# Kernel optimization log

Measured on AMD Instinct MI355X. Metric: run time of the kernel, lower is better.

The kernel has to match this reference:

```python
import jax, jax.numpy as jnp
import numpy as np

EMBED_DIM = 1024
NUM_HEADS = 16
HEAD_DIM = EMBED_DIM // NUM_HEADS


def setup_inputs() -> dict:
    key = jax.random.key(0)
    kx, kq, kk, kv, ko = jax.random.split(key, 5)
    B, S = 4, 2048
    std = 1.0 / np.sqrt(EMBED_DIM)
    x = jax.random.normal(kx, (B, S, EMBED_DIM), dtype=jnp.float32)
    # nn.Linear weights stored as [out, in]; applied as x @ W.T
    Wq = jax.random.normal(kq, (EMBED_DIM, EMBED_DIM), dtype=jnp.float32) * std
    Wk = jax.random.normal(kk, (EMBED_DIM, EMBED_DIM), dtype=jnp.float32) * std
    Wv = jax.random.normal(kv, (EMBED_DIM, EMBED_DIM), dtype=jnp.float32) * std
    Wo = jax.random.normal(ko, (EMBED_DIM, EMBED_DIM), dtype=jnp.float32) * std
    return {"x": x, "Wq": Wq, "Wk": Wk, "Wv": Wv, "Wo": Wo}


def reference(x, Wq, Wk, Wv, Wo):
    B, S, E = x.shape
    H, D = NUM_HEADS, HEAD_DIM
    scale = jnp.sqrt(jnp.float32(D))

    def proj(W):
        # x @ W.T -> (B, S, E) -> (B, H, S, D)
        return (x @ W.T).reshape(B, S, H, D).transpose(0, 2, 1, 3)

    q, k, v = proj(Wq), proj(Wk), proj(Wv)
    scores = jnp.einsum("bhsd,bhtd->bhst", q, k) / scale  # (B,H,S,S)
    causal = jnp.tril(jnp.ones((S, S), dtype=bool))
    scores = jnp.where(causal, scores, -jnp.inf)
    attn = jax.nn.softmax(scores, axis=-1)  # dropout in eval mode = identity
    out = jnp.einsum("bhst,bhtd->bhsd", attn, v)  # (B,H,S,D)
    out = out.transpose(0, 2, 1, 3).reshape(B, S, E)
    return out @ Wo.T
```

## Files before the change

kernel.cpp:

```cpp
#include <hip/hip_runtime.h>
#include <stdint.h>

#define NHEADS 16
#define EDIM   1024
#define SEQ    2048
#define BATCH  4

typedef float  floatx4 __attribute__((ext_vector_type(4)));
typedef __bf16 bf16x8  __attribute__((ext_vector_type(8)));
typedef unsigned short u16;

__device__ __forceinline__ u16 f2bf(float f) {
  union { float f; unsigned int u; } v; v.f = f;
  return (u16)((v.u + 0x7fffu + ((v.u >> 16) & 1u)) >> 16);
}

__device__ __forceinline__ unsigned int pkbf(float lo, float hi) {
  union { float f; unsigned int u; } a, c;
  a.f = lo; c.f = hi;
  return __builtin_amdgcn_perm(c.u + 0x8000u, a.u + 0x8000u, 0x07060302u);
}

__device__ __forceinline__ void gl2lds16(const u16* g, u16* l) {
  __builtin_amdgcn_global_load_lds(
      (const __attribute__((address_space(1))) unsigned int*)g,
      (__attribute__((address_space(3))) unsigned int*)l, 16, 0, 0);
}

__global__ void cvt_all(const float* __restrict__ x,  const float* __restrict__ wq,
                        const float* __restrict__ wk, const float* __restrict__ wv,
                        const float* __restrict__ wo, u16* __restrict__ xb,
                        u16* __restrict__ wqkv, u16* __restrict__ wob, float qscale) {
  const float* src; u16* dst; int n4; float sc = 1.f;
  switch (blockIdx.y) {
    case 0: src = x;  dst = xb;             n4 = 2097152; break;
    case 1: src = wq; dst = wqkv;           n4 = 262144; sc = qscale; break;
    case 2: src = wk; dst = wqkv + 1048576; n4 = 262144; break;
    case 3: src = wv; dst = wqkv + 2097152; n4 = 262144; break;
    default: src = wo; dst = wob;           n4 = 262144; break;
  }
  const int stride = gridDim.x * blockDim.x;
  for (int i = blockIdx.x * blockDim.x + threadIdx.x; i < n4; i += stride) {
    float4 f = ((const float4*)src)[i];
    uint2 o;
    o.x = pkbf(f.x * sc, f.y * sc);
    o.y = pkbf(f.z * sc, f.w * sc);
    ((uint2*)dst)[i] = o;
  }
}

template <int MODE>
__global__ __launch_bounds__(256, 2)
void gemm_tn(const u16* __restrict__ A, const u16* __restrict__ B,
             void* __restrict__ Cq, u16* __restrict__ Ck, u16* __restrict__ Cv,
             int Kdim) {
  __shared__ u16 As[128 * 64];
  __shared__ u16 Bs[128 * 64];
  const int tid  = threadIdx.x;
  const int w    = tid >> 6, lane = tid & 63;
  const int quad = lane >> 4, l15 = lane & 15;
  const int sr   = lane >> 3, sc8 = lane & 7;
  const int rowA0 = blockIdx.y * 128, rowB0 = blockIdx.x * 128;
  const int wrow  = (w >> 1) * 64,    wcol  = (w & 1) * 64;
  const int matid = (MODE == 0) ? (rowA0 >> 10) : 1;

  const floatx4 vzero = {0.f, 0.f, 0.f, 0.f};
  floatx4 acc[4][4];
#pragma unroll
  for (int mi = 0; mi < 4; ++mi)
#pragma unroll
    for (int ni = 0; ni < 4; ++ni) acc[mi][ni] = vzero;

  for (int k0 = 0; k0 < Kdim; k0 += 64) {
    __syncthreads();
#pragma unroll
    for (int i = 0; i < 4; ++i) {
      const int r = w * 32 + i * 8;
      gl2lds16(A + (size_t)(rowA0 + r + sr) * Kdim + k0 + ((sc8 ^ sr) * 8), As + r * 64);
      gl2lds16(B + (size_t)(rowB0 + r + sr) * Kdim + k0 + ((sc8 ^ sr) * 8), Bs + r * 64);
    }
    __syncthreads();
#pragma unroll
    for (int ks = 0; ks < 2; ++ks) {
      bf16x8 af[4], bfr[4];
#pragma unroll
      for (int mi = 0; mi < 4; ++mi)
        af[mi] = *(const bf16x8*)(As + (wrow + mi * 16 + l15) * 64 + (((ks * 4 + quad) ^ (l15 & 7)) * 8));
#pragma unroll
      for (int ni = 0; ni < 4; ++ni)
        bfr[ni] = *(const bf16x8*)(Bs + (wcol + ni * 16 + l15) * 64 + (((ks * 4 + quad) ^ (l15 & 7)) * 8));
      if (MODE == 0 && matid == 2) {
#pragma unroll
        for (int mi = 0; mi < 4; ++mi)
#pragma unroll
          for (int ni = 0; ni < 4; ++ni)
            acc[mi][ni] = __builtin_amdgcn_mfma_f32_16x16x32_bf16(bfr[ni], af[mi], acc[mi][ni], 0, 0, 0);
      } else {
#pragma unroll
        for (int mi = 0; mi < 4; ++mi)
#pragma unroll
          for (int ni = 0; ni < 4; ++ni)
            acc[mi][ni] = __builtin_amdgcn_mfma_f32_16x16x32_bf16(af[mi], bfr[ni], acc[mi][ni], 0, 0, 0);
      }
    }
  }

#pragma unroll
  for (int mi = 0; mi < 4; ++mi)
#pragma unroll
    for (int ni = 0; ni < 4; ++ni) {
      if (MODE == 1) {
        const int e0 = rowA0 + wrow + mi * 16 + quad * 4;
        const int s  = rowB0 + wcol + ni * 16 + l15;
        *(floatx4*)((float*)Cq + (size_t)s * 1024 + e0) = acc[mi][ni];
      } else if (matid < 2) {
        const int e0 = rowA0 + wrow + mi * 16 + quad * 4;
        const int s  = rowB0 + wcol + ni * 16 + l15;
        const int e_loc = e0 & 1023;
        u16* dst = (matid == 0) ? (u16*)Cq : Ck;
        uint2 pk;
        pk.x = pkbf(acc[mi][ni][0], acc[mi][ni][1]);
        pk.y = pkbf(acc[mi][ni][2], acc[mi][ni][3]);
        *(uint2*)(dst + (size_t)s * 1024 + e_loc) = pk;
      } else {
        const int e_loc = (rowA0 + wrow + mi * 16 + l15) & 1023;
        const int s_full = rowB0 + wcol + ni * 16 + quad * 4;
        const int bb = s_full >> 11, s_loc = s_full & 2047;
        uint2 pk;
        pk.x = pkbf(acc[mi][ni][0], acc[mi][ni][1]);
        pk.y = pkbf(acc[mi][ni][2], acc[mi][ni][3]);
        *(uint2*)(Cv + (size_t)(bb * 1024 + e_loc) * SEQ + s_loc) = pk;
      }
    }
}

__global__ __launch_bounds__(512, 4)
void attn_fwd(const u16* __restrict__ Q, const u16* __restrict__ K,
              const u16* __restrict__ Vt, u16* __restrict__ Ctx) {
  __shared__ u16 Ks[2][128 * 64];
  __shared__ u16 Vs[2][64 * 128];
  const int tid  = threadIdx.x;
  const int w    = tid >> 6, lane = tid & 63;
  const int quad = lane >> 4, l15 = lane & 15;
  const int bh = blockIdx.x, b = bh >> 4, h = bh & 15;
  const int p  = blockIdx.y;
  const int qts[2] = {p, 15 - p};
  const int kmax = qts[1];

  bf16x8 bq[2][2];
#pragma unroll
  for (int tt = 0; tt < 2; ++tt)
#pragma unroll
    for (int ks = 0; ks < 2; ++ks) {
      const int qs = qts[tt] * 128 + w * 16 + l15;
      bq[tt][ks] = *(const bf16x8*)(Q + (size_t)(b * SEQ + qs) * EDIM + h * 64 + ks * 32 + quad * 8);
    }

  const floatx4 vzero = {0.f, 0.f, 0.f, 0.f};
  floatx4 o_acc[2][4];
  float l_run[2] = {0.f, 0.f};
#pragma unroll
  for (int tt = 0; tt < 2; ++tt)
#pragma unroll
    for (int di = 0; di < 4; ++di) o_acc[tt][di] = vzero;

  const int krow = lane >> 3, kch = lane & 7;
  const int vrow = lane >> 4, vch = lane & 15;

#define STAGE_KV(buf, ktn)                                                          \
  {                                                                                 \
    _Pragma("unroll")                                                               \
    for (int ii = 0; ii < 2; ++ii) {                                                \
      const int r0 = w * 16 + ii * 8;                                               \
      const int row = r0 + krow;                                                    \
      gl2lds16(K + (size_t)(b * SEQ + (ktn) * 128 + row) * EDIM + h * 64 +          \
                   ((kch ^ (row & 7)) * 8),                                         \
               &Ks[buf][r0 * 64]);                                                  \
      const int d0 = w * 8 + ii * 4;                                                \
      const int dd = d0 + vrow;                                                     \
      gl2lds16(Vt + (size_t)(bh * 64 + dd) * SEQ + (ktn) * 128 +                    \
                   ((vch ^ (dd & 15)) * 8),                                         \
               &Vs[buf][d0 * 128]);                                                 \
    }                                                                               \
  }

  STAGE_KV(0, 0);

  for (int kt = 0; kt <= kmax; ++kt) {
    const int cur = kt & 1;
    __syncthreads();
    if (kt < kmax) STAGE_KV(cur ^ 1, kt + 1);
    const u16* Ksc = &Ks[cur][0];
    const u16* Vsc = &Vs[cur][0];

#pragma unroll
    for (int tt = 1; tt >= 0; --tt) {
      if (tt == 0 && kt > qts[0]) continue;

      floatx4 s_acc[8];
#pragma unroll
      for (int mi = 0; mi < 8; ++mi) s_acc[mi] = vzero;
#pragma unroll
      for (int ks = 0; ks < 2; ++ks) {
        bf16x8 ak[8];
#pragma unroll
        for (int mi = 0; mi < 8; ++mi)
          ak[mi] = *(const bf16x8*)(Ksc + (mi * 16 + l15) * 64 + (((ks * 4 + quad) ^ (l15 & 7)) * 8));
#pragma unroll
        for (int mi = 0; mi < 8; ++mi)
          s_acc[mi] = __builtin_amdgcn_mfma_f32_16x16x32_bf16(ak[mi], bq[tt][ks], s_acc[mi], 0, 0, 0);
      }

      if (kt == qts[tt]) {
        const int q_loc = w * 16 + l15;
#pragma unroll
        for (int mi = 0; mi < 8; ++mi)
#pragma unroll
          for (int r = 0; r < 4; ++r) {
            const int t_loc = mi * 16 + quad * 4 + r;
            if (t_loc > q_loc) s_acc[mi][r] = -1e30f;
          }
      }

      float ls = 0.f;
      unsigned int pk[4][4];
#pragma unroll
      for (int mi = 0; mi < 8; ++mi) {
        float p0 = __builtin_amdgcn_exp2f(s_acc[mi][0]);
        float p1 = __builtin_amdgcn_exp2f(s_acc[mi][1]);
        float p2 = __builtin_amdgcn_exp2f(s_acc[mi][2]);
        float p3 = __builtin_amdgcn_exp2f(s_acc[mi][3]);
        ls += (p0 + p1) + (p2 + p3);
        pk[mi >> 1][(mi & 1) * 2 + 0] = pkbf(p0, p1);
        pk[mi >> 1][(mi & 1) * 2 + 1] = pkbf(p2, p3);
      }
      ls += __shfl_xor(ls, 16, 64);
      ls += __shfl_xor(ls, 32, 64);
      l_run[tt] += ls;

#pragma unroll
      for (int ks = 0; ks < 4; ++ks) {
        union { unsigned int u[4]; bf16x8 v; } pb;
        pb.u[0] = pk[ks][0]; pb.u[1] = pk[ks][1];
        pb.u[2] = pk[ks][2]; pb.u[3] = pk[ks][3];
        const int cA = ((ks * 4 + (quad >> 1)) ^ l15) * 8 + (quad & 1) * 4;
        const int cB = ((ks * 4 + 2 + (quad >> 1)) ^ l15) * 8 + (quad & 1) * 4;
#pragma unroll
        for (int di = 0; di < 4; ++di) {
          const u16* vrowp = Vsc + (di * 16 + l15) * 128;
          union { uint2 u2[2]; bf16x8 v; } va;
          va.u2[0] = *(const uint2*)(vrowp + cA);
          va.u2[1] = *(const uint2*)(vrowp + cB);
          o_acc[tt][di] = __builtin_amdgcn_mfma_f32_16x16x32_bf16(va.v, pb.v, o_acc[tt][di], 0, 0, 0);
        }
      }
    }
  }

#pragma unroll
  for (int tt = 0; tt < 2; ++tt) {
    const float rl = 1.f / l_run[tt];
    const int qs = qts[tt] * 128 + w * 16 + l15;
#pragma unroll
    for (int di = 0; di < 4; ++di) {
      uint2 ov;
      ov.x = pkbf(o_acc[tt][di][0] * rl, o_acc[tt][di][1] * rl);
      ov.y = pkbf(o_acc[tt][di][2] * rl, o_acc[tt][di][3] * rl);
      *(uint2*)(Ctx + (size_t)(b * SEQ + qs) * EDIM + h * 64 + di * 16 + quad * 4) = ov;
    }
  }
#undef STAGE_KV
}

extern "C" void kernel_launch(void* const* d_in, const int* in_sizes, int n_in,
                              void* d_out, int out_size, void* d_ws, size_t ws_size,
                              hipStream_t stream) {
  const float* x  = (const float*)d_in[0];
  const float* Wq = (const float*)d_in[1];
  const float* Wk = (const float*)d_in[2];
  const float* Wv = (const float*)d_in[3];
  const float* Wo = (const float*)d_in[4];
  float* out = (float*)d_out;
  u16* ws = (u16*)d_ws;

  const size_t ME = (size_t)BATCH * SEQ * EDIM;
  u16* Xb   = ws;
  u16* Wqkv = Xb + ME;
  u16* Wob  = Wqkv + 3u * 1024 * 1024;
  u16* Qb   = Wob + 1024u * 1024;
  u16* Kb   = Qb + ME;
  u16* Vtr  = Kb + ME;
  u16* Ctx  = Vtr + ME;

  const float qscale = 0.125f * 1.44269504f;

  cvt_all<<<dim3(512, 5), 256, 0, stream>>>(x, Wq, Wk, Wv, Wo, Xb, Wqkv, Wob, qscale);
  gemm_tn<0><<<dim3(64, 24), 256, 0, stream>>>(Wqkv, Xb, (void*)Qb, Kb, Vtr, EDIM);
  attn_fwd<<<dim3(64, 8), 512, 0, stream>>>(Qb, Kb, Vtr, Ctx);
  gemm_tn<1><<<dim3(64, 8), 256, 0, stream>>>(Wob, Ctx, (void*)out, nullptr, nullptr, EDIM);
}
```

Measured before the change: 254.0 us.

## Share K fragments across paired query tiles and permute V layout for vector loads

The attention loop now processes both query tiles of a block in one pass over each K tile, loading K fragments once and issuing MFMAs for both tiles. The V projection is split into its own GEMM template mode, which writes V^T with a permuted sequence order so the PV stage can fetch one 16-byte LDS read instead of two 8-byte reads. The intent is less LDS traffic and more MFMA issue per load. In exchange, register pressure rises from holding two score sets and two packed probability sets, and there is one extra kernel launch.

```diff
diff --git a/kernel.cpp b/kernel.cpp
--- a/kernel.cpp
+++ b/kernel.cpp
@@ -62,7 +62,6 @@
   const int sr   = lane >> 3, sc8 = lane & 7;
   const int rowA0 = blockIdx.y * 128, rowB0 = blockIdx.x * 128;
   const int wrow  = (w >> 1) * 64,    wcol  = (w & 1) * 64;
-  const int matid = (MODE == 0) ? (rowA0 >> 10) : 1;
 
   const floatx4 vzero = {0.f, 0.f, 0.f, 0.f};
   floatx4 acc[4][4];
@@ -89,22 +88,19 @@
 #pragma unroll
       for (int ni = 0; ni < 4; ++ni)
         bfr[ni] = *(const bf16x8*)(Bs + (wcol + ni * 16 + l15) * 64 + (((ks * 4 + quad) ^ (l15 & 7)) * 8));
-      if (MODE == 0 && matid == 2) {
-#pragma unroll
-        for (int mi = 0; mi < 4; ++mi)
-#pragma unroll
-          for (int ni = 0; ni < 4; ++ni)
+#pragma unroll
+      for (int mi = 0; mi < 4; ++mi)
+#pragma unroll
+        for (int ni = 0; ni < 4; ++ni) {
+          if (MODE == 2)
             acc[mi][ni] = __builtin_amdgcn_mfma_f32_16x16x32_bf16(bfr[ni], af[mi], acc[mi][ni], 0, 0, 0);
-      } else {
-#pragma unroll
-        for (int mi = 0; mi < 4; ++mi)
-#pragma unroll
-          for (int ni = 0; ni < 4; ++ni)
+          else
             acc[mi][ni] = __builtin_amdgcn_mfma_f32_16x16x32_bf16(af[mi], bfr[ni], acc[mi][ni], 0, 0, 0);
-      }
-    }
-  }
-
+        }
+    }
+  }
+
+  const int matid = (MODE == 0) ? (rowA0 >> 10) : 0;
 #pragma unroll
   for (int mi = 0; mi < 4; ++mi)
 #pragma unroll
@@ -113,7 +109,7 @@
         const int e0 = rowA0 + wrow + mi * 16 + quad * 4;
         const int s  = rowB0 + wcol + ni * 16 + l15;
         *(floatx4*)((float*)Cq + (size_t)s * 1024 + e0) = acc[mi][ni];
-      } else if (matid < 2) {
+      } else if (MODE == 0) {
         const int e0 = rowA0 + wrow + mi * 16 + quad * 4;
         const int s  = rowB0 + wcol + ni * 16 + l15;
         const int e_loc = e0 & 1023;
@@ -123,20 +119,21 @@
         pk.y = pkbf(acc[mi][ni][2], acc[mi][ni][3]);
         *(uint2*)(dst + (size_t)s * 1024 + e_loc) = pk;
       } else {
-        const int e_loc = (rowA0 + wrow + mi * 16 + l15) & 1023;
+        const int e_loc = rowA0 + wrow + mi * 16 + l15;
         const int s_full = rowB0 + wcol + ni * 16 + quad * 4;
-        const int bb = s_full >> 11, s_loc = s_full & 2047;
+        const int pos = (s_full & ~31) | (quad << 3) | ((ni & 1) << 2);
+        const int bb = pos >> 11, pos_loc = pos & 2047;
         uint2 pk;
         pk.x = pkbf(acc[mi][ni][0], acc[mi][ni][1]);
         pk.y = pkbf(acc[mi][ni][2], acc[mi][ni][3]);
-        *(uint2*)(Cv + (size_t)(bb * 1024 + e_loc) * SEQ + s_loc) = pk;
+        *(uint2*)(Cv + (size_t)(bb * 1024 + e_loc) * SEQ + pos_loc) = pk;
       }
     }
 }
 
 __global__ __launch_bounds__(512, 4)
 void attn_fwd(const u16* __restrict__ Q, const u16* __restrict__ K,
-              const u16* __restrict__ Vt, u16* __restrict__ Ctx) {
+              const u16* __restrict__ Vp, u16* __restrict__ Ctx) {
   __shared__ u16 Ks[2][128 * 64];
   __shared__ u16 Vs[2][64 * 128];
   const int tid  = threadIdx.x;
@@ -178,7 +175,7 @@
                &Ks[buf][r0 * 64]);                                                  \
       const int d0 = w * 8 + ii * 4;                                                \
       const int dd = d0 + vrow;                                                     \
-      gl2lds16(Vt + (size_t)(bh * 64 + dd) * SEQ + (ktn) * 128 +                    \
+      gl2lds16(Vp + (size_t)(bh * 64 + dd) * SEQ + (ktn) * 128 +                    \
                    ((vch ^ (dd & 15)) * 8),                                         \
                &Vs[buf][d0 * 128]);                                                 \
     }                                                                               \
@@ -192,67 +189,100 @@
     if (kt < kmax) STAGE_KV(cur ^ 1, kt + 1);
     const u16* Ksc = &Ks[cur][0];
     const u16* Vsc = &Vs[cur][0];
-
-#pragma unroll
-    for (int tt = 1; tt >= 0; --tt) {
-      if (tt == 0 && kt > qts[0]) continue;
-
-      floatx4 s_acc[8];
-#pragma unroll
-      for (int mi = 0; mi < 8; ++mi) s_acc[mi] = vzero;
+    const bool dual = (kt <= qts[0]);
+
+    float ls1 = 0.f, ls0 = 0.f;
+    unsigned int pk1[4][4], pk0[4][4];
+#pragma unroll
+    for (int hf = 0; hf < 2; ++hf) {
+      floatx4 s1[4], s0[4];
+#pragma unroll
+      for (int mi = 0; mi < 4; ++mi) { s1[mi] = vzero; s0[mi] = vzero; }
 #pragma unroll
       for (int ks = 0; ks < 2; ++ks) {
-        bf16x8 ak[8];
-#pragma unroll
-        for (int mi = 0; mi < 8; ++mi)
-          ak[mi] = *(const bf16x8*)(Ksc + (mi * 16 + l15) * 64 + (((ks * 4 + quad) ^ (l15 & 7)) * 8));
-#pragma unroll
-        for (int mi = 0; mi < 8; ++mi)
-          s_acc[mi] = __builtin_amdgcn_mfma_f32_16x16x32_bf16(ak[mi], bq[tt][ks], s_acc[mi], 0, 0, 0);
-      }
-
-      if (kt == qts[tt]) {
-        const int q_loc = w * 16 + l15;
-#pragma unroll
-        for (int mi = 0; mi < 8; ++mi)
+        bf16x8 ak[4];
+#pragma unroll
+        for (int mi = 0; mi < 4; ++mi)
+          ak[mi] = *(const bf16x8*)(Ksc + ((hf * 4 + mi) * 16 + l15) * 64 + (((ks * 4 + quad) ^ (l15 & 7)) * 8));
+#pragma unroll
+        for (int mi = 0; mi < 4; ++mi)
+          s1[mi] = __builtin_amdgcn_mfma_f32_16x16x32_bf16(ak[mi], bq[1][ks], s1[mi], 0, 0, 0);
+        if (dual) {
+#pragma unroll
+          for (int mi = 0; mi < 4; ++mi)
+            s0[mi] = __builtin_amdgcn_mfma_f32_16x16x32_bf16(ak[mi], bq[0][ks], s0[mi], 0, 0, 0);
+        }
+      }
+      const int q_loc = w * 16 + l15;
+      if (kt == qts[1]) {
+#pragma unroll
+        for (int mi = 0; mi < 4; ++mi)
 #pragma unroll
           for (int r = 0; r < 4; ++r) {
-            const int t_loc = mi * 16 + quad * 4 + r;
-            if (t_loc > q_loc) s_acc[mi][r] = -1e30f;
+            const int t_loc = (hf * 4 + mi) * 16 + quad * 4 + r;
+            if (t_loc > q_loc) s1[mi][r] = -1e30f;
           }
       }
-
-      float ls = 0.f;
-      unsigned int pk[4][4];
-#pragma unroll
-      for (int mi = 0; mi < 8; ++mi) {
-        float p0 = __builtin_amdgcn_exp2f(s_acc[mi][0]);
-        float p1 = __builtin_amdgcn_exp2f(s_acc[mi][1]);
-        float p2 = __builtin_amdgcn_exp2f(s_acc[mi][2]);
-        float p3 = __builtin_amdgcn_exp2f(s_acc[mi][3]);
-        ls += (p0 + p1) + (p2 + p3);
-        pk[mi >> 1][(mi & 1) * 2 + 0] = pkbf(p0, p1);
-        pk[mi >> 1][(mi & 1) * 2 + 1] = pkbf(p2, p3);
-      }
-      ls += __shfl_xor(ls, 16, 64);
-      ls += __shfl_xor(ls, 32, 64);
-      l_run[tt] += ls;
-
-#pragma unroll
-      for (int ks = 0; ks < 4; ++ks) {
-        union { unsigned int u[4]; bf16x8 v; } pb;
-        pb.u[0] = pk[ks][0]; pb.u[1] = pk[ks][1];
-        pb.u[2] = pk[ks][2]; pb.u[3] = pk[ks][3];
-        const int cA = ((ks * 4 + (quad >> 1)) ^ l15) * 8 + (quad & 1) * 4;
-        const int cB = ((ks * 4 + 2 + (quad >> 1)) ^ l15) * 8 + (quad & 1) * 4;
-#pragma unroll
-        for (int di = 0; di < 4; ++di) {
-          const u16* vrowp = Vsc + (di * 16 + l15) * 128;
-          union { uint2 u2[2]; bf16x8 v; } va;
-          va.u2[0] = *(const uint2*)(vrowp + cA);
-          va.u2[1] = *(const uint2*)(vrowp + cB);
-          o_acc[tt][di] = __builtin_amdgcn_mfma_f32_16x16x32_bf16(va.v, pb.v, o_acc[tt][di], 0, 0, 0);
+      if (dual && kt == qts[0]) {
+#pragma unroll
+        for (int mi = 0; mi < 4; ++mi)
+#pragma unroll
+          for (int r = 0; r < 4; ++r) {
+            const int t_loc = (hf * 4 + mi) * 16 + quad * 4 + r;
+            if (t_loc > q_loc) s0[mi][r] = -1e30f;
+          }
+      }
+#pragma unroll
+      for (int mi = 0; mi < 4; ++mi) {
+        const int g = hf * 4 + mi;
+        {
+          float p0 = __builtin_amdgcn_exp2f(s1[mi][0]);
+          float p1 = __builtin_amdgcn_exp2f(s1[mi][1]);
+          float p2 = __builtin_amdgcn_exp2f(s1[mi][2]);
+          float p3 = __builtin_amdgcn_exp2f(s1[mi][3]);
+          ls1 += (p0 + p1) + (p2 + p3);
+          pk1[g >> 1][(g & 1) * 2 + 0] = pkbf(p0, p1);
+          pk1[g >> 1][(g & 1) * 2 + 1] = pkbf(p2, p3);
         }
+        if (dual) {
+          float p0 = __builtin_amdgcn_exp2f(s0[mi][0]);
+          float p1 = __builtin_amdgcn_exp2f(s0[mi][1]);
+          float p2 = __builtin_amdgcn_exp2f(s0[mi][2]);
+          float p3 = __builtin_amdgcn_exp2f(s0[mi][3]);
+          ls0 += (p0 + p1) + (p2 + p3);
+          pk0[g >> 1][(g & 1) * 2 + 0] = pkbf(p0, p1);
+          pk0[g >> 1][(g & 1) * 2 + 1] = pkbf(p2, p3);
+        }
+      }
+    }
+    ls1 += __shfl_xor(ls1, 16, 64);
+    ls1 += __shfl_xor(ls1, 32, 64);
+    l_run[1] += ls1;
+    if (dual) {
+      ls0 += __shfl_xor(ls0, 16, 64);
+      ls0 += __shfl_xor(ls0, 32, 64);
+      l_run[0] += ls0;
+    }
+
+#pragma unroll
+    for (int ks = 0; ks < 4; ++ks) {
+      bf16x8 va[4];
+#pragma unroll
+      for (int di = 0; di < 4; ++di)
+        va[di] = *(const bf16x8*)(Vsc + (di * 16 + l15) * 128 + (((ks * 4 + quad) ^ l15) * 8));
+      union { unsigned int u[4]; bf16x8 v; } pb1;
+      pb1.u[0] = pk1[ks][0]; pb1.u[1] = pk1[ks][1];
+      pb1.u[2] = pk1[ks][2]; pb1.u[3] = pk1[ks][3];
+#pragma unroll
+      for (int di = 0; di < 4; ++di)
+        o_acc[1][di] = __builtin_amdgcn_mfma_f32_16x16x32_bf16(va[di], pb1.v, o_acc[1][di], 0, 0, 0);
+      if (dual) {
+        union { unsigned int u[4]; bf16x8 v; } pb0;
+        pb0.u[0] = pk0[ks][0]; pb0.u[1] = pk0[ks][1];
+        pb0.u[2] = pk0[ks][2]; pb0.u[3] = pk0[ks][3];
+#pragma unroll
+        for (int di = 0; di < 4; ++di)
+          o_acc[0][di] = __builtin_amdgcn_mfma_f32_16x16x32_bf16(va[di], pb0.v, o_acc[0][di], 0, 0, 0);
       }
     }
   }
@@ -289,13 +319,14 @@
   u16* Wob  = Wqkv + 3u * 1024 * 1024;
   u16* Qb   = Wob + 1024u * 1024;
   u16* Kb   = Qb + ME;
-  u16* Vtr  = Kb + ME;
-  u16* Ctx  = Vtr + ME;
+  u16* Vpb  = Kb + ME;
+  u16* Ctx  = Vpb + ME;
 
   const float qscale = 0.125f * 1.44269504f;
 
   cvt_all<<<dim3(512, 5), 256, 0, stream>>>(x, Wq, Wk, Wv, Wo, Xb, Wqkv, Wob, qscale);
-  gemm_tn<0><<<dim3(64, 24), 256, 0, stream>>>(Wqkv, Xb, (void*)Qb, Kb, Vtr, EDIM);
-  attn_fwd<<<dim3(64, 8), 512, 0, stream>>>(Qb, Kb, Vtr, Ctx);
+  gemm_tn<0><<<dim3(64, 16), 256, 0, stream>>>(Wqkv, Xb, (void*)Qb, Kb, nullptr, EDIM);
+  gemm_tn<2><<<dim3(64, 8), 256, 0, stream>>>(Wqkv + 2u * 1048576, Xb, nullptr, nullptr, Vpb, EDIM);
+  attn_fwd<<<dim3(64, 8), 512, 0, stream>>>(Qb, Kb, Vpb, Ctx);
   gemm_tn<1><<<dim3(64, 8), 256, 0, stream>>>(Wob, Ctx, (void*)out, nullptr, nullptr, EDIM);
 }
```

New measurement: 314.7 us. 23.9% more time.
